# Kernel tuning notes

Measured on AMD Instinct MI355X. Metric: run time of the kernel, lower is better.

## Reference

```python
import jax, jax.numpy as jnp
import numpy as np

B, NH, T, D = 2, 16, 2048, 64

def setup_inputs() -> dict:
    key = jax.random.key(0)
    kq, kk, kv = jax.random.split(key, 3)
    Q = jax.random.normal(kq, (B, NH, T, D), dtype=jnp.float32)
    K = jax.random.normal(kk, (B, NH, T, D), dtype=jnp.float32)
    V = jax.random.normal(kv, (B, NH, T, D), dtype=jnp.float32)
    return {"Q": Q, "K": K, "V": V}

def reference(Q, K, V):
    # scores: [B, nh, T, T]
    Dh = Q.shape[-1]
    scale = 1.0 / jnp.sqrt(jnp.asarray(Dh, Q.dtype))
    scores = jnp.einsum('bhtd,bhsd->bhts', Q, K) * scale
    Tq = Q.shape[2]
    causal = jnp.tril(jnp.ones((Tq, Tq), dtype=bool))
    scores = jnp.where(causal, scores, jnp.asarray(-jnp.inf, scores.dtype))
    attn = jax.nn.softmax(scores, axis=-1)
    return jnp.einsum('bhts,bhsd->bhtd', attn, V)
```

## Files before the change

kernel.cpp:

```cpp
#include <hip/hip_runtime.h>
#include <hip/hip_bf16.h>


typedef __bf16 bf16;
typedef __bf16 bf16x4 __attribute__((ext_vector_type(4)));
typedef __bf16 bf16x8 __attribute__((ext_vector_type(8)));
typedef float floatx4 __attribute__((ext_vector_type(4)));

#define T_SEQ 2048
#define DH 64
#define TKS 32
#define BHN 32
#define CEXP 0.18033688011112042f

__device__ __forceinline__ void gload16(const bf16* g, bf16* l) {
    __builtin_amdgcn_global_load_lds(
        (const __attribute__((address_space(1))) void*)g,
        (__attribute__((address_space(3))) void*)l, 16, 0, 0);
}

__global__ __launch_bounds__(256) void prep(const float* __restrict__ K,
                                            const float* __restrict__ V,
                                            bf16* __restrict__ Kb,
                                            bf16* __restrict__ Vt) {
    const int bid = (int)blockIdx.x;
    const int tid = (int)threadIdx.x;
    if (bid < 512) {
        size_t i = ((size_t)bid * 256 + tid) * 8;
        #pragma unroll
        for (int it = 0; it < 4; ++it) {
            float4 a = *(const float4*)(K + i + 0);
            float4 b = *(const float4*)(K + i + 4);
            bf16x8 o;
            o[0]=(bf16)a.x; o[1]=(bf16)a.y; o[2]=(bf16)a.z; o[3]=(bf16)a.w;
            o[4]=(bf16)b.x; o[5]=(bf16)b.y; o[6]=(bf16)b.z; o[7]=(bf16)b.w;
            *(bf16x8*)(Kb + i) = o;
            i += (size_t)512 * 256 * 8;
        }
        return;
    }
    __shared__ bf16 tile[2][64][72];
    const int vb = bid - 512;
    const int bh = vb & (BHN - 1);
    const int tp = (vb >> 5) * 128;
    #pragma unroll
    for (int tt = 0; tt < 2; ++tt) {
        const int r = tid >> 2;
        const int c = (tid & 3) * 16;
        const float* s = V + ((size_t)bh * T_SEQ + tp + tt * 64 + r) * DH + c;
        float4 f0 = *(const float4*)(s + 0);
        float4 f1 = *(const float4*)(s + 4);
        float4 f2 = *(const float4*)(s + 8);
        float4 f3 = *(const float4*)(s + 12);
        bf16x8 p0, p1;
        p0[0]=(bf16)f0.x; p0[1]=(bf16)f0.y; p0[2]=(bf16)f0.z; p0[3]=(bf16)f0.w;
        p0[4]=(bf16)f1.x; p0[5]=(bf16)f1.y; p0[6]=(bf16)f1.z; p0[7]=(bf16)f1.w;
        p1[0]=(bf16)f2.x; p1[1]=(bf16)f2.y; p1[2]=(bf16)f2.z; p1[3]=(bf16)f2.w;
        p1[4]=(bf16)f3.x; p1[5]=(bf16)f3.y; p1[6]=(bf16)f3.z; p1[7]=(bf16)f3.w;
        *(bf16x8*)&tile[tt][r][c + 0] = p0;
        *(bf16x8*)&tile[tt][r][c + 8] = p1;
    }
    __syncthreads();
    #pragma unroll
    for (int tt = 0; tt < 2; ++tt) {
        const int d   = tid >> 2;
        const int tch = (tid & 3) * 16;
        bf16x8 o0, o1;
        #pragma unroll
        for (int j = 0; j < 8; ++j) { o0[j] = tile[tt][tch + j][d]; o1[j] = tile[tt][tch + 8 + j][d]; }
        bf16* o = Vt + ((size_t)bh * DH + d) * T_SEQ + tp + tt * 64 + tch;
        *(bf16x8*)(o + 0) = o0;
        *(bf16x8*)(o + 8) = o1;
    }
}

__global__ __launch_bounds__(256, 2)
void fa_fwd(const float* __restrict__ Qg, const bf16* __restrict__ Kb,
            const bf16* __restrict__ Vt, float* __restrict__ Og)
{
    __shared__ __align__(16) bf16 smem[32768];

    const int gid = (int)blockIdx.x;
    const int bh  = gid & (BHN - 1);
    const int m   = gid >> 5;
    const int B   = 64 - 2 * m;
    const int qh  = (31 - m) * 64;
    const int ql  = m * 64;

    const int tid  = (int)threadIdx.x;
    const int wave = tid >> 6;
    const int lane = tid & 63;
    const int quad = lane >> 4;
    const int l16  = lane & 15;
    const int psw  = (l16 >> 1) & 3;

    const int tw0 = (wave < 2) ? wave * 17 : 34 + (wave - 2) * 16;
    const int tw1 = tw0 + ((wave < 2) ? 17 : 16);

    bf16* W = smem + wave * 8192;

    const bf16* Kbh = Kb + (size_t)bh * (T_SEQ * DH);
    const bf16* Vbh = Vt + (size_t)bh * (DH * T_SEQ);
    const size_t qrb = (size_t)bh * T_SEQ;

    const int rl  = lane >> 3;
    const int kch = (lane & 7) ^ (rl & 7);
    const int vr  = lane >> 2;
    const int vch = (lane & 3) ^ ((lane >> 3) & 3);

    bool heavyNow = (tw0 < B);
    int  qbase    = heavyNow ? qh : ql;
    bool hasPark  = false;

    bf16x8 qb[4][2];
    auto loadQ = [&](int qb0) {
        #pragma unroll
        for (int nt = 0; nt < 4; ++nt) {
            const int qrow = qb0 + nt * 16 + l16;
            #pragma unroll
            for (int kk = 0; kk < 2; ++kk) {
                const float* s = Qg + (qrb + qrow) * DH + kk * 32 + quad * 8;
                float4 f0 = *(const float4*)(s);
                float4 f1 = *(const float4*)(s + 4);
                bf16x8 t;
                t[0]=(bf16)f0.x; t[1]=(bf16)f0.y; t[2]=(bf16)f0.z; t[3]=(bf16)f0.w;
                t[4]=(bf16)f1.x; t[5]=(bf16)f1.y; t[6]=(bf16)f1.z; t[7]=(bf16)f1.w;
                qb[nt][kk] = t;
            }
        }
    };
    loadQ(qbase);

    floatx4 oacc[4][4];
    #pragma unroll
    for (int mt = 0; mt < 4; ++mt)
        #pragma unroll
        for (int nt = 0; nt < 4; ++nt) oacc[mt][nt] = (floatx4){0.f,0.f,0.f,0.f};
    float lpart[4] = {0.f, 0.f, 0.f, 0.f};
    bf16x4 parked[16];
    #pragma unroll
    for (int f = 0; f < 16; ++f) parked[f] = (bf16x4){(bf16)0.f,(bf16)0.f,(bf16)0.f,(bf16)0.f};
    float lpark[4] = {0.f, 0.f, 0.f, 0.f};

    auto kTileOf = [&](int t) { return (t < B) ? t : (t - B); };

    auto stageK = [&](int kt, bf16* dst) {
        const bf16* kg = Kbh + (size_t)kt * TKS * DH;
        #pragma unroll
        for (int g = 0; g < 4; ++g)
            gload16(kg + (size_t)(g * 8 + rl) * DH + kch * 8, dst + g * 512);
    };
    auto stageV = [&](int kt, bf16* dst) {
        const bf16* vg = Vbh + kt * TKS;
        #pragma unroll
        for (int g = 0; g < 4; ++g)
            gload16(vg + (size_t)(g * 16 + vr) * T_SEQ + vch * 8, dst + g * 512);
    };

    stageK(kTileOf(tw0), W);
    stageV(kTileOf(tw0), W + 4096);

    for (int t = tw0; t < tw1; ++t) {
        if (heavyNow && t == B) {
            #pragma unroll
            for (int f = 0; f < 16; ++f) {
                bf16x4 w;
                #pragma unroll
                for (int e = 0; e < 4; ++e) w[e] = (bf16)oacc[f >> 2][f & 3][e];
                parked[f] = w;
            }
            #pragma unroll
            for (int nt = 0; nt < 4; ++nt) { lpark[nt] = lpart[nt]; lpart[nt] = 0.f; }
            #pragma unroll
            for (int mt = 0; mt < 4; ++mt)
                #pragma unroll
                for (int nt = 0; nt < 4; ++nt) oacc[mt][nt] = (floatx4){0.f,0.f,0.f,0.f};
            hasPark = true;
            heavyNow = false;
            qbase = ql;
            loadQ(ql);
        }

        const int cur = (t - tw0) & 1;
        bf16* Kcur = W + cur * 2048;
        bf16* Vcur = W + 4096 + cur * 2048;
        bf16* Pw   = Kcur;
        const int kt = kTileOf(t);
        const int k0 = kt * TKS;

        const bool pf = (t + 1 < tw1);
        if (pf) {
            const int ktn = kTileOf(t + 1);
            stageK(ktn, W + (cur ^ 1) * 2048);
            stageV(ktn, W + 4096 + (cur ^ 1) * 2048);
            __builtin_amdgcn_s_waitcnt(0x0F78);
        } else {
            __builtin_amdgcn_s_waitcnt(0x0F70);
        }

        floatx4 sa[2][4];
        #pragma unroll
        for (int mt = 0; mt < 2; ++mt)
            #pragma unroll
            for (int nt = 0; nt < 4; ++nt) sa[mt][nt] = (floatx4){0.f,0.f,0.f,0.f};
        #pragma unroll
        for (int kk = 0; kk < 2; ++kk) {
            #pragma unroll
            for (int mt = 0; mt < 2; ++mt) {
                bf16x8 kf = *(const bf16x8*)&Kcur[(mt * 16 + l16) * 64 + (((kk * 4 + quad) ^ (l16 & 7)) * 8)];
                #pragma unroll
                for (int nt = 0; nt < 4; ++nt)
                    sa[mt][nt] = __builtin_amdgcn_mfma_f32_16x16x32_bf16(kf, qb[nt][kk], sa[mt][nt], 0, 0, 0);
            }
        }
        if (k0 + TKS - 1 > qbase) {
            #pragma unroll
            for (int mt = 0; mt < 2; ++mt)
                #pragma unroll
                for (int nt = 0; nt < 4; ++nt) {
                    const int qg = qbase + nt * 16 + l16;
                    #pragma unroll
                    for (int r = 0; r < 4; ++r) {
                        const int keyg = k0 + mt * 16 + quad * 4 + r;
                        if (keyg > qg) sa[mt][nt][r] = -INFINITY;
                    }
                }
        }
        #pragma unroll
        for (int mt = 0; mt < 2; ++mt)
            #pragma unroll
            for (int nt = 0; nt < 4; ++nt) {
                bf16x4 w;
                #pragma unroll
                for (int r = 0; r < 4; ++r) {
                    const float pv = __builtin_amdgcn_exp2f(CEXP * sa[mt][nt][r]);
                    lpart[nt] += pv;
                    w[r] = (bf16)pv;
                }
                const int slot = (mt * 2 + (quad >> 1)) ^ psw;
                *(bf16x4*)&Pw[(nt * 16 + l16) * 32 + slot * 8 + (quad & 1) * 4] = w;
            }
        bf16x8 pfr[4];
        #pragma unroll
        for (int nt = 0; nt < 4; ++nt)
            pfr[nt] = *(const bf16x8*)&Pw[(nt * 16 + l16) * 32 + ((quad ^ psw) * 8)];
        #pragma unroll
        for (int mt = 0; mt < 4; ++mt) {
            bf16x8 vf = *(const bf16x8*)&Vcur[(mt * 16 + l16) * 32 + ((quad ^ psw) * 8)];
            #pragma unroll
            for (int nt = 0; nt < 4; ++nt)
                oacc[mt][nt] = __builtin_amdgcn_mfma_f32_16x16x32_bf16(vf, pfr[nt], oacc[mt][nt], 0, 0, 0);
        }
    }

    __syncthreads();
    const bool hH = (tw0 < B);
    const bool hL = (tw1 > B);
    if (wave >= 1 && hH) {
        bf16* a = smem + (wave - 1) * 4608;
        float* al = (float*)(a + 4096);
        #pragma unroll
        for (int f = 0; f < 16; ++f) {
            bf16x4 w;
            if (hasPark) w = parked[f];
            else {
                #pragma unroll
                for (int e = 0; e < 4; ++e) w[e] = (bf16)oacc[f >> 2][f & 3][e];
            }
            *(bf16x4*)&a[(f * 64 + lane) * 4] = w;
        }
        #pragma unroll
        for (int nt = 0; nt < 4; ++nt)
            al[nt * 64 + lane] = hasPark ? lpark[nt] : lpart[nt];
    }
    if (wave >= 2 && hL) {
        bf16* a = smem + (wave + 1) * 4608;
        float* al = (float*)(a + 4096);
        #pragma unroll
        for (int f = 0; f < 16; ++f) {
            bf16x4 w;
            #pragma unroll
            for (int e = 0; e < 4; ++e) w[e] = (bf16)oacc[f >> 2][f & 3][e];
            *(bf16x4*)&a[(f * 64 + lane) * 4] = w;
        }
        #pragma unroll
        for (int nt = 0; nt < 4; ++nt)
            al[nt * 64 + lane] = lpart[nt];
    }
    __syncthreads();

    if (wave <= 1) {
        int qfin;
        if (wave == 0) {
            qfin = qh;
            const int nA = (B > 50) ? 3 : ((B > 34) ? 2 : 1);
            for (int i = 0; i < nA; ++i) {
                const bf16* a = smem + i * 4608;
                const float* al = (const float*)(a + 4096);
                #pragma unroll
                for (int f = 0; f < 16; ++f) {
                    bf16x4 w = *(const bf16x4*)&a[(f * 64 + lane) * 4];
                    #pragma unroll
                    for (int e = 0; e < 4; ++e) oacc[f >> 2][f & 3][e] += (float)w[e];
                }
                #pragma unroll
                for (int nt = 0; nt < 4; ++nt) lpart[nt] += al[nt * 64 + lane];
            }
        } else {
            qfin = ql;
            #pragma unroll
            for (int mt = 0; mt < 4; ++mt)
                #pragma unroll
                for (int nt = 0; nt < 4; ++nt) oacc[mt][nt] = (floatx4){0.f,0.f,0.f,0.f};
            #pragma unroll
            for (int nt = 0; nt < 4; ++nt) lpart[nt] = 0.f;
            const int i0 = (B < 50) ? 3 : 4;
            for (int i = i0; i <= 4; ++i) {
                const bf16* a = smem + i * 4608;
                const float* al = (const float*)(a + 4096);
                #pragma unroll
                for (int f = 0; f < 16; ++f) {
                    bf16x4 w = *(const bf16x4*)&a[(f * 64 + lane) * 4];
                    #pragma unroll
                    for (int e = 0; e < 4; ++e) oacc[f >> 2][f & 3][e] += (float)w[e];
                }
                #pragma unroll
                for (int nt = 0; nt < 4; ++nt) lpart[nt] += al[nt * 64 + lane];
            }
        }
        float invl[4];
        #pragma unroll
        for (int nt = 0; nt < 4; ++nt) {
            float v = lpart[nt];
            v += __shfl_xor(v, 16);
            v += __shfl_xor(v, 32);
            invl[nt] = 1.0f / v;
        }
        #pragma unroll
        for (int nt = 0; nt < 4; ++nt) {
            const size_t qrow = qrb + qfin + nt * 16 + l16;
            #pragma unroll
            for (int mt = 0; mt < 4; ++mt) {
                float4 o;
                o.x = oacc[mt][nt][0] * invl[nt];
                o.y = oacc[mt][nt][1] * invl[nt];
                o.z = oacc[mt][nt][2] * invl[nt];
                o.w = oacc[mt][nt][3] * invl[nt];
                *(float4*)&Og[qrow * DH + mt * 16 + quad * 4] = o;
            }
        }
    }
}

extern "C" void kernel_launch(void* const* d_in, const int* in_sizes, int n_in,
                              void* d_out, int out_size, void* d_ws, size_t ws_size,
                              hipStream_t stream) {
    const float* Q = (const float*)d_in[0];
    const float* K = (const float*)d_in[1];
    const float* V = (const float*)d_in[2];
    float* O = (float*)d_out;
    (void)in_sizes; (void)n_in; (void)out_size; (void)ws_size;

    const size_t nelem = (size_t)BHN * T_SEQ * DH;
    bf16* Kbf = (bf16*)d_ws;
    bf16* Vtb = Kbf + nelem;

    prep<<<dim3(1024), dim3(256), 0, stream>>>(K, V, Kbf, Vtb);
    fa_fwd<<<dim3(512), dim3(256), 0, stream>>>(Q, Kbf, Vtb, O);
}
```

Baseline: 123.8 us.

## Split key tiles across six waves, single-buffer V, fold exp scale into K

Raises the block from 4 to 6 waves, each handling 11 key tiles instead of 16-17, so each query-block pair's work is spread over more waves. V staging becomes single-buffered: V fragments are read into registers before the next V tile is staged into the same buffer, which frees LDS to fit six waves. The softmax exp2 scale constant is folded into K during the bf16 conversion, removing a multiply per score. The cross-wave reduction is generalized to the new partition, at the cost of more partial results to merge and a shorter V prefetch window.

Result: slower. 209.5 us (+69.1%).

```diff
diff --git a/kernel.cpp b/kernel.cpp
--- a/kernel.cpp
+++ b/kernel.cpp
@@ -32,8 +32,8 @@
             float4 a = *(const float4*)(K + i + 0);
             float4 b = *(const float4*)(K + i + 4);
             bf16x8 o;
-            o[0]=(bf16)a.x; o[1]=(bf16)a.y; o[2]=(bf16)a.z; o[3]=(bf16)a.w;
-            o[4]=(bf16)b.x; o[5]=(bf16)b.y; o[6]=(bf16)b.z; o[7]=(bf16)b.w;
+            o[0]=(bf16)(a.x*CEXP); o[1]=(bf16)(a.y*CEXP); o[2]=(bf16)(a.z*CEXP); o[3]=(bf16)(a.w*CEXP);
+            o[4]=(bf16)(b.x*CEXP); o[5]=(bf16)(b.y*CEXP); o[6]=(bf16)(b.z*CEXP); o[7]=(bf16)(b.w*CEXP);
             *(bf16x8*)(Kb + i) = o;
             i += (size_t)512 * 256 * 8;
         }
@@ -74,11 +74,11 @@
     }
 }
 
-__global__ __launch_bounds__(256, 2)
+__global__ __launch_bounds__(384, 3)
 void fa_fwd(const float* __restrict__ Qg, const bf16* __restrict__ Kb,
             const bf16* __restrict__ Vt, float* __restrict__ Og)
 {
-    __shared__ __align__(16) bf16 smem[32768];
+    __shared__ __align__(16) bf16 smem[36864];
 
     const int gid = (int)blockIdx.x;
     const int bh  = gid & (BHN - 1);
@@ -94,10 +94,10 @@
     const int l16  = lane & 15;
     const int psw  = (l16 >> 1) & 3;
 
-    const int tw0 = (wave < 2) ? wave * 17 : 34 + (wave - 2) * 16;
-    const int tw1 = tw0 + ((wave < 2) ? 17 : 16);
-
-    bf16* W = smem + wave * 8192;
+    const int tw0 = wave * 11;
+    const int tw1 = tw0 + 11;
+
+    bf16* W = smem + wave * 6144;
 
     const bf16* Kbh = Kb + (size_t)bh * (T_SEQ * DH);
     const bf16* Vbh = Vt + (size_t)bh * (DH * T_SEQ);
@@ -183,16 +183,14 @@
 
         const int cur = (t - tw0) & 1;
         bf16* Kcur = W + cur * 2048;
-        bf16* Vcur = W + 4096 + cur * 2048;
+        bf16* Vcur = W + 4096;
         bf16* Pw   = Kcur;
         const int kt = kTileOf(t);
         const int k0 = kt * TKS;
 
         const bool pf = (t + 1 < tw1);
         if (pf) {
-            const int ktn = kTileOf(t + 1);
-            stageK(ktn, W + (cur ^ 1) * 2048);
-            stageV(ktn, W + 4096 + (cur ^ 1) * 2048);
+            stageK(kTileOf(t + 1), W + (cur ^ 1) * 2048);
             __builtin_amdgcn_s_waitcnt(0x0F78);
         } else {
             __builtin_amdgcn_s_waitcnt(0x0F70);
@@ -233,7 +231,7 @@
                 bf16x4 w;
                 #pragma unroll
                 for (int r = 0; r < 4; ++r) {
-                    const float pv = __builtin_amdgcn_exp2f(CEXP * sa[mt][nt][r]);
+                    const float pv = __builtin_amdgcn_exp2f(sa[mt][nt][r]);
                     lpart[nt] += pv;
                     w[r] = (bf16)pv;
                 }
@@ -244,16 +242,26 @@
         #pragma unroll
         for (int nt = 0; nt < 4; ++nt)
             pfr[nt] = *(const bf16x8*)&Pw[(nt * 16 + l16) * 32 + ((quad ^ psw) * 8)];
+        if (pf) __builtin_amdgcn_s_waitcnt(0x0F74);
+        bf16x8 vf[4];
+        #pragma unroll
+        for (int mt = 0; mt < 4; ++mt)
+            vf[mt] = *(const bf16x8*)&Vcur[(mt * 16 + l16) * 32 + ((quad ^ psw) * 8)];
+        if (pf) {
+            __builtin_amdgcn_s_waitcnt(0xC07F);
+            stageV(kTileOf(t + 1), Vcur);
+        }
         #pragma unroll
         for (int mt = 0; mt < 4; ++mt) {
-            bf16x8 vf = *(const bf16x8*)&Vcur[(mt * 16 + l16) * 32 + ((quad ^ psw) * 8)];
             #pragma unroll
             for (int nt = 0; nt < 4; ++nt)
-                oacc[mt][nt] = __builtin_amdgcn_mfma_f32_16x16x32_bf16(vf, pfr[nt], oacc[mt][nt], 0, 0, 0);
+                oacc[mt][nt] = __builtin_amdgcn_mfma_f32_16x16x32_bf16(vf[mt], pfr[nt], oacc[mt][nt], 0, 0, 0);
         }
     }
 
     __syncthreads();
+    const int nH = (B + 10) / 11;
+    const int wc = B / 11;
     const bool hH = (tw0 < B);
     const bool hL = (tw1 > B);
     if (wave >= 1 && hH) {
@@ -273,8 +281,8 @@
         for (int nt = 0; nt < 4; ++nt)
             al[nt * 64 + lane] = hasPark ? lpark[nt] : lpart[nt];
     }
-    if (wave >= 2 && hL) {
-        bf16* a = smem + (wave + 1) * 4608;
+    if (hL) {
+        bf16* a = smem + (nH - 1 + wave - wc) * 4608;
         float* al = (float*)(a + 4096);
         #pragma unroll
         for (int f = 0; f < 16; ++f) {
@@ -290,43 +298,29 @@
     __syncthreads();
 
     if (wave <= 1) {
-        int qfin;
+        int qfin, i0, i1;
         if (wave == 0) {
-            qfin = qh;
-            const int nA = (B > 50) ? 3 : ((B > 34) ? 2 : 1);
-            for (int i = 0; i < nA; ++i) {
-                const bf16* a = smem + i * 4608;
-                const float* al = (const float*)(a + 4096);
-                #pragma unroll
-                for (int f = 0; f < 16; ++f) {
-                    bf16x4 w = *(const bf16x4*)&a[(f * 64 + lane) * 4];
-                    #pragma unroll
-                    for (int e = 0; e < 4; ++e) oacc[f >> 2][f & 3][e] += (float)w[e];
-                }
-                #pragma unroll
-                for (int nt = 0; nt < 4; ++nt) lpart[nt] += al[nt * 64 + lane];
-            }
+            qfin = qh; i0 = 0; i1 = nH - 1;
         } else {
-            qfin = ql;
+            qfin = ql; i0 = nH - 1; i1 = nH - 1 + (6 - wc);
             #pragma unroll
             for (int mt = 0; mt < 4; ++mt)
                 #pragma unroll
                 for (int nt = 0; nt < 4; ++nt) oacc[mt][nt] = (floatx4){0.f,0.f,0.f,0.f};
             #pragma unroll
             for (int nt = 0; nt < 4; ++nt) lpart[nt] = 0.f;
-            const int i0 = (B < 50) ? 3 : 4;
-            for (int i = i0; i <= 4; ++i) {
-                const bf16* a = smem + i * 4608;
-                const float* al = (const float*)(a + 4096);
-                #pragma unroll
-                for (int f = 0; f < 16; ++f) {
-                    bf16x4 w = *(const bf16x4*)&a[(f * 64 + lane) * 4];
-                    #pragma unroll
-                    for (int e = 0; e < 4; ++e) oacc[f >> 2][f & 3][e] += (float)w[e];
-                }
-                #pragma unroll
-                for (int nt = 0; nt < 4; ++nt) lpart[nt] += al[nt * 64 + lane];
-            }
+        }
+        for (int i = i0; i < i1; ++i) {
+            const bf16* a = smem + i * 4608;
+            const float* al = (const float*)(a + 4096);
+            #pragma unroll
+            for (int f = 0; f < 16; ++f) {
+                bf16x4 w = *(const bf16x4*)&a[(f * 64 + lane) * 4];
+                #pragma unroll
+                for (int e = 0; e < 4; ++e) oacc[f >> 2][f & 3][e] += (float)w[e];
+            }
+            #pragma unroll
+            for (int nt = 0; nt < 4; ++nt) lpart[nt] += al[nt * 64 + lane];
         }
         float invl[4];
         #pragma unroll
@@ -366,5 +360,5 @@
     bf16* Vtb = Kbf + nelem;
 
     prep<<<dim3(1024), dim3(256), 0, stream>>>(K, V, Kbf, Vtb);
-    fa_fwd<<<dim3(512), dim3(256), 0, stream>>>(Q, Kbf, Vtb, O);
+    fa_fwd<<<dim3(512), dim3(384), 0, stream>>>(Q, Kbf, Vtb, O);
 }
```
